# Performance work log

Hardware: AMD Instinct MI355X
Metric: run time of the kernel (lower is better)

## Reference

```python
import jax, jax.numpy as jnp
import numpy as np

B, CLS, C, H, HP, WP, K = 16, 20, 512, 4, 32, 32, 9
G = H * CLS  # grapher channels = 80
EPS = 1e-5
BNS = 1.0 / np.sqrt(1.0 + EPS)  # eval-mode BN, running_mean=0, running_var=1


def _bn(x, g, b, axis):
    shape = [1] * x.ndim
    shape[axis] = -1
    return x * (g * BNS).reshape(shape) + b.reshape(shape)


def setup_inputs():
    key = jax.random.key(0)
    ks = jax.random.split(key, 16)
    def rn(k, shp, scale=0.02):
        return jax.random.normal(k, shp, dtype=jnp.float32) * scale
    return {
        "x_cls": jax.random.normal(ks[0], (B, CLS, C), jnp.float32),
        "x_patch": jax.random.normal(ks[1], (B, C, HP, WP), jnp.float32),
        "norm_x_w": jnp.ones((C, 1, 1), jnp.float32),
        "norm_x_b": jnp.zeros((C, 1, 1), jnp.float32),
        "pq_w": rn(ks[2], (C, C)), "pq_b": rn(ks[3], (C,)),
        "ncls_w": jnp.ones((C,), jnp.float32), "ncls_b": jnp.zeros((C,), jnp.float32),
        "pkv_w": rn(ks[4], (2 * C, C)), "pkv_b": rn(ks[5], (2 * C,)),
        "fc1_w": rn(ks[6], (G, G)), "fc1_b": rn(ks[7], (G,)),
        "bn1_g": jnp.ones((G,), jnp.float32), "bn1_b": jnp.zeros((G,), jnp.float32),
        "mr_w": rn(ks[8], (2 * G, 2 * G // H)), "mr_b": rn(ks[9], (2 * G,)),
        "bn2_g": jnp.ones((2 * G,), jnp.float32), "bn2_b": jnp.zeros((2 * G,), jnp.float32),
        "fc2_w": rn(ks[10], (G, 2 * G)), "fc2_b": rn(ks[11], (G,)),
        "bn3_g": jnp.ones((G,), jnp.float32), "bn3_b": jnp.zeros((G,), jnp.float32),
        "proj_w": rn(ks[12], (C, C)), "proj_b": rn(ks[13], (C,)),
    }


def _forward(x_cls, x_patch, norm_x_w, norm_x_b, pq_w, pq_b, ncls_w, ncls_b,
             pkv_w, pkv_b, fc1_w, fc1_b, bn1_g, bn1_b, mr_w, mr_b, bn2_g, bn2_b,
             fc2_w, fc2_b, bn3_g, bn3_b, proj_w, proj_b):
    hd = C // H
    N = HP * WP
    scale = hd ** -0.5
    # norm_x: LayerNormGeneral over (C,H,W)
    c0 = x_patch - x_patch.mean(axis=(1, 2, 3), keepdims=True)
    s0 = (c0 * c0).mean(axis=(1, 2, 3), keepdims=True)
    xn = c0 / jnp.sqrt(s0 + EPS) * norm_x_w + norm_x_b
    # proj_q (1x1 conv) -> multi-head query [B,H,N,hd]
    q = jnp.einsum('oc,bchw->bohw', pq_w, xn) + pq_b[None, :, None, None]
    q = q.reshape(B, H, hd, N).transpose(0, 1, 3, 2)
    # norm_cls: LayerNorm over channel dim
    m = x_cls.mean(-1, keepdims=True)
    v = ((x_cls - m) ** 2).mean(-1, keepdims=True)
    xc = (x_cls - m) / jnp.sqrt(v + EPS) * ncls_w + ncls_b
    kv = xc @ pkv_w.T + pkv_b                                  # [B,Cls,2C]
    k_, v_ = kv[..., :C], kv[..., C:]
    key_ = k_.reshape(B, CLS, H, hd).transpose(0, 2, 3, 1)     # [B,H,hd,Cls]
    val = v_.reshape(B, CLS, H, hd).transpose(0, 2, 1, 3)      # [B,H,Cls,hd]
    attn = jnp.einsum('bhnd,bhdc->bhnc', q, key_) * scale      # [B,H,N,Cls]
    amap = attn.reshape(B, H, HP, WP, CLS).transpose(0, 1, 4, 2, 3).reshape(B, G, HP, WP)
    # ---- Grapher (ViG gcn_lib): fc1 -> DyGraphConv(MRConv, KNN) -> fc2 -> residual ----
    sc = amap
    x = jnp.einsum('oc,bchw->bohw', fc1_w, amap) + fc1_b[None, :, None, None]
    x = _bn(x, bn1_g, bn1_b, 1)
    xf = x.reshape(B, G, N).transpose(0, 2, 1)                 # [B,N,G]
    # dense KNN on L2-normalized features (indices only, non-diff)
    xu = xf / jnp.maximum(jnp.linalg.norm(xf, axis=-1, keepdims=True), 1e-12)
    sq = jnp.sum(xu * xu, axis=-1)                             # [B,N]
    neg_d = 2.0 * jnp.einsum('bnc,bmc->bnm', xu, xu) - sq[:, :, None] - sq[:, None, :]
    _, nn_idx = jax.lax.top_k(neg_d, K)                        # [B,N,K]
    neigh = xf[jnp.arange(B)[:, None, None], nn_idx]           # [B,N,K,G]
    xj = jnp.max(neigh - xf[:, :, None, :], axis=2)            # [B,N,G] max-relative
    y = jnp.stack([xf, xj], axis=-1).reshape(B, N, 2 * G)      # interleave (x0,xj0,x1,...)
    # grouped 1x1 conv (groups=H), BN, GELU
    yg = y.reshape(B, N, H, 2 * G // H)
    wg = mr_w.reshape(H, 2 * G // H, 2 * G // H)
    z = jnp.einsum('bngi,goi->bngo', yg, wg).reshape(B, N, 2 * G) + mr_b
    z = _bn(z, bn2_g, bn2_b, 2)
    z = jax.nn.gelu(z, approximate=False)
    z2 = z @ fc2_w.T + fc2_b                                   # [B,N,G]
    z2 = _bn(z2, bn3_g, bn3_b, 2)
    gout = z2.transpose(0, 2, 1).reshape(B, G, HP, WP) + sc
    # ---- softmax-weighted value aggregation ----
    attn2 = gout.reshape(B, H, CLS, N).transpose(0, 1, 3, 2)   # [B,H,N,Cls]
    attn2 = jax.nn.softmax(attn2, axis=-1)
    out = jnp.einsum('bhnc,bhcd->bhnd', attn2, val)            # [B,H,N,hd]
    out = out.transpose(0, 1, 3, 2).reshape(B, C, HP, WP)
    out = jnp.einsum('oc,bchw->bohw', proj_w, out) + proj_b[None, :, None, None]
    return x_patch + out


def reference(x_cls, x_patch, norm_x_w, norm_x_b, pq_w, pq_b, ncls_w, ncls_b,
              pkv_w, pkv_b, fc1_w, fc1_b, bn1_g, bn1_b, mr_w, mr_b, bn2_g, bn2_b,
              fc2_w, fc2_b, bn3_g, bn3_b, proj_w, proj_b):
    return _forward(x_cls, x_patch, norm_x_w, norm_x_b, pq_w, pq_b, ncls_w, ncls_b,
                    pkv_w, pkv_b, fc1_w, fc1_b, bn1_g, bn1_b, mr_w, mr_b, bn2_g, bn2_b,
                    fc2_w, fc2_b, bn3_g, bn3_b, proj_w, proj_b)
```

## Files before the change

kernel.cpp:

```cpp
#include <hip/hip_runtime.h>
#include <math.h>

#define DI __device__ __forceinline__

constexpr int B_ = 16, CLS_ = 20, C_ = 512, H_ = 4, HD_ = 128, N_ = 1024, G_ = 80, G2_ = 160, K_ = 9;
constexpr float EPS_ = 1e-5f;
constexpr float BNS_ = 0.9999950000374997f;
constexpr float SCALE_ = 0.08838834764831845f;
constexpr float INVSQRT2_ = 0.7071067811865475f;

typedef __attribute__((ext_vector_type(8))) short bf16x8;
typedef __attribute__((ext_vector_type(4))) float f32x4;

constexpr long OFF_PART  = 0;
constexpr long OFF_STATS = 2048;
constexpr long OFF_EB    = 4096;
constexpr long OFF_EBB   = OFF_EB    + 524288;
constexpr long OFF_KV    = OFF_EBB   + 2048;
constexpr long OFF_AMAPT = OFF_KV    + 327680;
constexpr long OFF_XF    = OFF_AMAPT + 1310720;
constexpr long OFF_XUB   = OFF_XF    + 1310720;
constexpr long OFF_W1BD  = OFF_XUB   + 786432;
constexpr long OFF_FC2B  = OFF_W1BD  + 16384;
constexpr long OFF_SQ    = OFF_FC2B  + 8192;
constexpr long OFF_NEGD  = OFF_SQ    + 16384;
constexpr long OFF_IDX   = OFF_NEGD  + 16777216;
constexpr long OFF_GOUTT = OFF_IDX   + 147456;
constexpr long OFF_WPB   = OFF_GOUTT + 1310720;
constexpr long OFF_Y     = OFF_WPB   + 131072;
constexpr long OFF_AMAPB = OFF_Y     + 1310720;
constexpr long OFF_FC1B  = OFF_AMAPB + 786432;

DI float wsum(float v){
#pragma unroll
  for(int d=1; d<64; d<<=1) v += __shfl_xor(v, d);
  return v;
}
DI unsigned short f2b(float f){
  unsigned u = __float_as_uint(f);
  unsigned r = (u + 0x7FFFu + ((u >> 16) & 1u)) >> 16;
  return (unsigned short)r;
}

#define GLOAD16(g, s) __builtin_amdgcn_global_load_lds((const __attribute__((address_space(1))) void*)(g), \
                        (__attribute__((address_space(3))) void*)(s), 16, 0, 0)

__global__ __launch_bounds__(256) void k_stats_partial(const float* __restrict__ x, float* __restrict__ part){
  int blk = blockIdx.x;
  const float4* xp = (const float4*)x;
  long base4 = (long)blk * 2048;
  int t = threadIdx.x;
  float s = 0.f, ss = 0.f;
#pragma unroll
  for(int j=0;j<8;++j){
    float4 v = xp[base4 + t + 256*j];
    s  += v.x + v.y + v.z + v.w;
    ss += v.x*v.x + v.y*v.y + v.z*v.z + v.w*v.w;
  }
  s = wsum(s); ss = wsum(ss);
  __shared__ float rs[4], rss[4];
  int wv = t >> 6;
  if((t & 63) == 0){ rs[wv] = s; rss[wv] = ss; }
  __syncthreads();
  if(t == 0){
    part[blk*2]   = rs[0]+rs[1]+rs[2]+rs[3];
    part[blk*2+1] = rss[0]+rss[1]+rss[2]+rss[3];
  }
}

__global__ __launch_bounds__(64) void k_stats_final(const float* __restrict__ part, float* __restrict__ stats){
  int b = blockIdx.x, t = threadIdx.x;
  float s  = part[(b*64+t)*2];
  float ss = part[(b*64+t)*2+1];
  s = wsum(s); ss = wsum(ss);
  if(t == 0){
    const float cnt = (float)(C_ * N_);
    float m = s / cnt;
    float var = ss / cnt - m*m;
    stats[b*2]   = m;
    stats[b*2+1] = 1.0f / sqrtf(var + EPS_);
  }
}

__global__ __launch_bounds__(256) void k_xn_t(const float* __restrict__ x, const float* __restrict__ stats,
                                              const float* __restrict__ nw, const float* __restrict__ nb,
                                              unsigned short* __restrict__ xnb){
  __shared__ float tile[64][65];
  int b = blockIdx.z, c0 = blockIdx.y*64, n0 = blockIdx.x*64;
  float m = stats[b*2], inv = stats[b*2+1];
  int t = threadIdx.x;
  const float* xb = x + ((long)b*C_ + c0)*N_ + n0;
#pragma unroll
  for(int j=0;j<4;++j){
    int idx = t + 256*j;
    int r = idx >> 4, c4 = (idx & 15)*4;
    float a = inv * nw[c0+r];
    float bb = nb[c0+r] - m*a;
    float4 v = *(const float4*)&xb[(long)r*N_ + c4];
    tile[r][c4]   = v.x*a + bb;
    tile[r][c4+1] = v.y*a + bb;
    tile[r][c4+2] = v.z*a + bb;
    tile[r][c4+3] = v.w*a + bb;
  }
  __syncthreads();
  unsigned short* ob = xnb + ((long)b*N_ + n0)*C_ + c0;
#pragma unroll
  for(int j=0;j<8;++j){
    int idx = t + 256*j;
    int n = idx >> 5, cc = (idx & 31)*2;
    ushort2 u;
    u.x = f2b(tile[cc][n]);
    u.y = f2b(tile[cc+1][n]);
    *(ushort2*)&ob[(long)n*C_ + cc] = u;
  }
}

__global__ __launch_bounds__(256) void k_wconv(const float* __restrict__ a, unsigned short* __restrict__ oa){
  long i = (long)blockIdx.x*256 + threadIdx.x;
  float4 v = ((const float4*)a)[i];
  uint2 o;
  o.x = (unsigned)f2b(v.x) | ((unsigned)f2b(v.y) << 16);
  o.y = (unsigned)f2b(v.z) | ((unsigned)f2b(v.w) << 16);
  ((uint2*)oa)[i] = o;
}

__global__ __launch_bounds__(256) void k_wsmall(const float* __restrict__ mrw, const float* __restrict__ fc2w,
                                                const float* __restrict__ fc1w,
                                                unsigned short* __restrict__ w1bd, unsigned short* __restrict__ fc2b16,
                                                unsigned short* __restrict__ fc1b16){
  int row = blockIdx.x, t = threadIdx.x;
  if(row < 160){
    if(t < 160){
      unsigned short v = 0;
      if(t/40 == row/40) v = f2b(mrw[row*40 + (t % 40)]);
      w1bd[row*160 + t] = v;
    }
  } else if(row < 240){
    if(t < 160) fc2b16[(row-160)*160 + t] = f2b(fc2w[(long)(row-160)*160 + t]);
  } else {
    int r = row - 240;
    if(t < 96) fc1b16[r*96 + t] = (t < G_) ? f2b(fc1w[(long)r*G_ + t]) : (unsigned short)0;
  }
}

__global__ __launch_bounds__(256) void k_eprep(const float* __restrict__ kv, const float* __restrict__ pqw,
                                               const float* __restrict__ pqb,
                                               unsigned short* __restrict__ Eb, float* __restrict__ ebb){
  int b = blockIdx.x, hh = blockIdx.y, cch = blockIdx.z, t = threadIdx.x;
  if(hh == 4){
    if(cch == 0){
      unsigned* z = (unsigned*)(Eb + ((long)b*128 + 80)*512);
      for(int i=t; i<12288; i+=256) z[i] = 0;
    }
    return;
  }
  int h = hh, c0 = cch*64;
  __shared__ float key[CLS_][HD_];
  __shared__ float part[4][CLS_][64];
  for(int i=t; i<CLS_*HD_; i+=256){
    int cls = i >> 7, d = i & 127;
    key[cls][d] = kv[((long)b*CLS_+cls)*1024 + h*HD_ + d];
  }
  __syncthreads();
  int c = t & 63, ds = t >> 6;
  float acc[CLS_] = {};
  const float* wp = pqw + ((long)(h*HD_ + ds*32))*C_ + c0 + c;
#pragma unroll 8
  for(int di=0; di<32; ++di){
    float wv = wp[(long)di*C_];
#pragma unroll
    for(int cls=0; cls<CLS_; ++cls) acc[cls] += key[cls][ds*32+di]*wv;
  }
#pragma unroll
  for(int cls=0; cls<CLS_; ++cls) part[ds][cls][c] = acc[cls];
  __syncthreads();
  for(int i=t; i<CLS_*64; i+=256){
    int cls = i >> 6, cc = i & 63;
    float v = part[0][cls][cc]+part[1][cls][cc]+part[2][cls][cc]+part[3][cls][cc];
    Eb[((long)b*128 + h*CLS_ + cls)*512 + c0 + cc] = f2b(v*SCALE_);
  }
  if(cch == 0 && t < CLS_){
    float bacc = 0.f;
    for(int d=0; d<HD_; ++d) bacc += key[t][d]*pqb[h*HD_+d];
    ebb[b*G_ + h*CLS_ + t] = bacc*SCALE_;
  }
}

__global__ __launch_bounds__(256) void k_amap_gemm(const unsigned short* __restrict__ Eb,
                                                   const unsigned short* __restrict__ Xb,
                                                   const float* __restrict__ ebb,
                                                   float* __restrict__ amapT,
                                                   unsigned short* __restrict__ amapb){
  __shared__ unsigned short Anl[2048];
  __shared__ unsigned short Bgl[4096];
  int b = blockIdx.y, n0 = blockIdx.x*64;
  int t = threadIdx.x, w = t >> 6, l = t & 63;
  int wr = w >> 1, wc = w & 1;
  f32x4 acc[2][4] = {};
  const unsigned short* At = Xb + ((long)b*N_ + n0 + w*16 + (l>>2))*512 + (l&3)*8;
  const unsigned short* Bt = Eb + ((long)b*128 + w*16 + (l>>2))*512 + (l&3)*8;
  int ra = wr*32 + (l & 15);
  int rb = wc*64 + (l & 15);
  int kq = (l >> 4) * 8;
  for(int k0 = 0; k0 < 512; k0 += 32){
    if(k0) __syncthreads();
    GLOAD16(At + k0,          &Anl[w*512]);
    GLOAD16(Bt + k0,          &Bgl[w*512]);
    GLOAD16(Bt + 64*512 + k0, &Bgl[2048 + w*512]);
    __syncthreads();
    bf16x8 af[2], bfr[4];
#pragma unroll
    for(int rt=0; rt<2; ++rt) af[rt]  = *(const bf16x8*)&Anl[(ra + rt*16)*32 + kq];
#pragma unroll
    for(int ct=0; ct<4; ++ct) bfr[ct] = *(const bf16x8*)&Bgl[(rb + ct*16)*32 + kq];
#pragma unroll
    for(int rt=0; rt<2; ++rt)
#pragma unroll
      for(int ct=0; ct<4; ++ct)
        acc[rt][ct] = __builtin_amdgcn_mfma_f32_16x16x32_bf16(af[rt], bfr[ct], acc[rt][ct], 0, 0, 0);
  }
  int r0 = (l >> 4)*4;
#pragma unroll
  for(int rt=0; rt<2; ++rt){
#pragma unroll
    for(int r=0; r<4; ++r){
      int n = n0 + wr*32 + rt*16 + r0 + r;
      long rowb  = ((long)b*N_ + n)*G_;
      long rowb9 = ((long)b*N_ + n)*96;
#pragma unroll
      for(int ct=0; ct<4; ++ct){
        int g = wc*64 + ct*16 + (l & 15);
        if(g < G_){
          float val = acc[rt][ct][r] + ebb[b*G_ + g];
          amapT[rowb + g] = val;
          amapb[rowb9 + g] = f2b(val);
        } else if(g < 96){
          amapb[rowb9 + g] = 0;
        }
      }
    }
  }
}

template<bool RES>
__global__ __launch_bounds__(256) void k_gemm_mfma(const unsigned short* __restrict__ Wb,
                                                   const unsigned short* __restrict__ Xb,
                                                   const float* __restrict__ bias,
                                                   const float* __restrict__ Res,
                                                   float* __restrict__ Out){
  __shared__ unsigned short Al[4096];
  __shared__ unsigned short Bl[4096];
  int b = blockIdx.z;
  int o0 = blockIdx.y*128, n0 = blockIdx.x*128;
  int t = threadIdx.x, w = t >> 6, l = t & 63;
  int wr = w >> 1, wc = w & 1;
  f32x4 acc[4][4] = {};
  const unsigned short* Wt = Wb + (long)(o0 + w*16 + (l>>2))*512 + (l&3)*8;
  const unsigned short* Xt = Xb + ((long)b*N_ + n0 + w*16 + (l>>2))*512 + (l&3)*8;
  int ra = wr*64 + (l & 15);
  int rb = wc*64 + (l & 15);
  int kq = (l >> 4) * 8;
  for(int k0 = 0; k0 < 512; k0 += 32){
    if(k0) __syncthreads();
    GLOAD16(Wt + k0,            &Al[w*512]);
    GLOAD16(Wt + 64*512 + k0,   &Al[2048 + w*512]);
    GLOAD16(Xt + k0,            &Bl[w*512]);
    GLOAD16(Xt + 64*512 + k0,   &Bl[2048 + w*512]);
    __syncthreads();
    bf16x8 af[4], bfr[4];
#pragma unroll
    for(int i=0;i<4;++i){
      af[i]  = *(const bf16x8*)&Al[(ra + i*16)*32 + kq];
      bfr[i] = *(const bf16x8*)&Bl[(rb + i*16)*32 + kq];
    }
#pragma unroll
    for(int mi=0; mi<4; ++mi)
#pragma unroll
      for(int ni=0; ni<4; ++ni)
        acc[mi][ni] = __builtin_amdgcn_mfma_f32_16x16x32_bf16(af[mi], bfr[ni], acc[mi][ni], 0, 0, 0);
  }
  long obase = ((long)b*C_ + o0 + wr*64)*N_ + n0 + wc*64 + (l & 15);
  int r0 = (l >> 4) * 4;
#pragma unroll
  for(int mi=0; mi<4; ++mi){
#pragma unroll
    for(int r=0; r<4; ++r){
      int row = mi*16 + r0 + r;
      float bi = bias[o0 + wr*64 + row];
#pragma unroll
      for(int ni=0; ni<4; ++ni){
        long oi = obase + (long)row*N_ + ni*16;
        float v = acc[mi][ni][r] + bi;
        if(RES) v += Res[oi];
        Out[oi] = v;
      }
    }
  }
}

__global__ __launch_bounds__(256) void k_cls_kv(const float* __restrict__ xcls,
                                                const float* __restrict__ ncw, const float* __restrict__ ncb,
                                                const float* __restrict__ pkvw, const float* __restrict__ pkvb,
                                                float* __restrict__ kv){
  int b = blockIdx.x;
  int ochunk = blockIdx.y;
  __shared__ float xc[CLS_][C_];
  int t = threadIdx.x, wv = t >> 6, l = t & 63;
  for(int cls = wv; cls < CLS_; cls += 4){
    const float* xr = xcls + ((long)b*CLS_ + cls) * C_;
    float vals[8];
    float s = 0.f, ss = 0.f;
#pragma unroll
    for(int j=0;j<8;++j){ float v = xr[l + 64*j]; vals[j] = v; s += v; ss += v*v; }
    s = wsum(s); ss = wsum(ss);
    float m = s / (float)C_;
    float var = ss / (float)C_ - m*m;
    float inv = 1.0f / sqrtf(var + EPS_);
#pragma unroll
    for(int j=0;j<8;++j){
      int c = l + 64*j;
      xc[cls][c] = (vals[j]-m)*inv*ncw[c] + ncb[c];
    }
  }
  __syncthreads();
  int o = ochunk*128 + (t & 127);
  int cls0 = (t >> 7) * 10;
  float acc[10] = {};
  const float* wrow = pkvw + (long)o * C_;
  for(int k4 = 0; k4 < C_; k4 += 4){
    float4 w4 = *(const float4*)&wrow[k4];
#pragma unroll
    for(int i=0;i<10;++i){
      acc[i] += w4.x*xc[cls0+i][k4] + w4.y*xc[cls0+i][k4+1] + w4.z*xc[cls0+i][k4+2] + w4.w*xc[cls0+i][k4+3];
    }
  }
  float bo = pkvb[o];
#pragma unroll
  for(int i=0;i<10;++i) kv[((long)b*CLS_ + cls0+i)*1024 + o] = acc[i] + bo;
}

__global__ __launch_bounds__(256) void k_fc1_mfma(const unsigned short* __restrict__ amapb,
                                                  const unsigned short* __restrict__ w1b,
                                                  const float* __restrict__ bias,
                                                  const float* __restrict__ g1, const float* __restrict__ b1,
                                                  float* __restrict__ xf, unsigned short* __restrict__ xub,
                                                  float* __restrict__ sq){
  int t = threadIdx.x, w = t >> 6, l = t & 63;
  long row0 = ((long)blockIdx.x*4 + w)*16;
  int lr = l & 15, lk = l >> 4;
  bf16x8 ay[3];
  const unsigned short* arow = amapb + (row0 + lr)*96 + lk*8;
#pragma unroll
  for(int ks=0; ks<3; ++ks) ay[ks] = *(const bf16x8*)&arow[ks*32];
  f32x4 acc[5] = {};
  const unsigned short* wrow = w1b + (long)lr*96 + lk*8;
#pragma unroll
  for(int ks=0; ks<3; ++ks){
#pragma unroll
    for(int ct=0; ct<5; ++ct){
      bf16x8 bw = *(const bf16x8*)&wrow[ct*16*96 + ks*32];
      acc[ct] = __builtin_amdgcn_mfma_f32_16x16x32_bf16(ay[ks], bw, acc[ct], 0, 0, 0);
    }
  }
  float v[5][4];
  float ssq[4] = {0.f,0.f,0.f,0.f};
#pragma unroll
  for(int ct=0; ct<5; ++ct){
    int o = ct*16 + lr;
    float bi = bias[o], ga = g1[o]*BNS_, bb = b1[o];
#pragma unroll
    for(int i=0;i<4;++i){
      float vv = (acc[ct][i] + bi)*ga + bb;
      v[ct][i] = vv;
      ssq[i] += vv*vv;
    }
  }
#pragma unroll
  for(int d=1; d<16; d<<=1){
#pragma unroll
    for(int i=0;i<4;++i) ssq[i] += __shfl_xor(ssq[i], d);
  }
#pragma unroll
  for(int i=0;i<4;++i){
    long row = row0 + lk*4 + i;
    float invn = 1.0f / fmaxf(sqrtf(ssq[i]), 1e-12f);
#pragma unroll
    for(int ct=0; ct<5; ++ct){
      int o = ct*16 + lr;
      xf[row*G_ + o] = v[ct][i];
      xub[row*96 + o] = f2b(v[ct][i]*invn);
    }
    xub[row*96 + 80 + lr] = 0;
    if(lr == 0) sq[row] = ssq[i]*invn*invn;
  }
}

__global__ __launch_bounds__(256) void k_negd_mfma(const unsigned short* __restrict__ xub,
                                                   const float* __restrict__ sq,
                                                   float* __restrict__ negd){
  __shared__ unsigned short Al[128*96];
  __shared__ unsigned short Bl[128*96];
  int b = blockIdx.z;
  int n0 = blockIdx.y*128, m0 = blockIdx.x*128;
  int t = threadIdx.x, w = t >> 6, l = t & 63;
  int wr = w >> 1, wc = w & 1;
  const unsigned short* gA = xub + ((long)b*N_ + n0)*96;
  const unsigned short* gB = xub + ((long)b*N_ + m0)*96;
#pragma unroll
  for(int rd=0; rd<6; ++rd){
    int chunk = rd*4 + w;
    GLOAD16(gA + chunk*512 + l*8, &Al[chunk*512]);
    GLOAD16(gB + chunk*512 + l*8, &Bl[chunk*512]);
  }
  __syncthreads();
  f32x4 acc[4][4] = {};
  int ra = wr*64 + (l & 15);
  int rb = wc*64 + (l & 15);
#pragma unroll
  for(int ks=0; ks<3; ++ks){
    int kq = ks*32 + (l >> 4)*8;
    bf16x8 af[4], bfr[4];
#pragma unroll
    for(int i=0;i<4;++i){
      af[i]  = *(const bf16x8*)&Al[(ra + i*16)*96 + kq];
      bfr[i] = *(const bf16x8*)&Bl[(rb + i*16)*96 + kq];
    }
#pragma unroll
    for(int mi=0; mi<4; ++mi)
#pragma unroll
      for(int ni=0; ni<4; ++ni)
        acc[mi][ni] = __builtin_amdgcn_mfma_f32_16x16x32_bf16(af[mi], bfr[ni], acc[mi][ni], 0, 0, 0);
  }
  int r0 = (l >> 4)*4;
  const float* sqb = sq + (long)b*N_;
#pragma unroll
  for(int mi=0; mi<4; ++mi){
#pragma unroll
    for(int r=0; r<4; ++r){
      int n = n0 + wr*64 + mi*16 + r0 + r;
      float sn = sqb[n];
      long row = ((long)b*N_ + n)*N_;
#pragma unroll
      for(int ni=0; ni<4; ++ni){
        int m = m0 + wc*64 + ni*16 + (l & 15);
        negd[row + m] = 2.f*acc[mi][ni][r] - sn - sqb[m];
      }
    }
  }
}

__global__ __launch_bounds__(256) void k_topk(const float* __restrict__ negd, int* __restrict__ idx){
  int t = threadIdx.x, wv = t >> 6, l = t & 63;
  long r = (long)blockIdx.x*4 + wv;
  const float* row = negd + r*N_;
  float vals[16];
#pragma unroll
  for(int j=0;j<16;++j) vals[j] = row[l + 64*j];
#pragma unroll
  for(int p=0; p<K_; ++p){
    float bv = vals[0]; int bj = 0;
#pragma unroll
    for(int j=1;j<16;++j) if(vals[j] > bv){ bv = vals[j]; bj = j; }
    int bm = l + 64*bj;
#pragma unroll
    for(int d=1; d<64; d<<=1){
      float ov = __shfl_xor(bv, d);
      int   om = __shfl_xor(bm, d);
      if(ov > bv || (ov == bv && om < bm)){ bv = ov; bm = om; }
    }
#pragma unroll
    for(int j=0;j<16;++j) if(bm == l + 64*j) vals[j] = -INFINITY;
    if(l == 0) idx[r*K_ + p] = bm;
  }
}

__global__ __launch_bounds__(256) void k_y(const float* __restrict__ xf, const int* __restrict__ idx,
                                           unsigned short* __restrict__ y){
  int t = threadIdx.x, wv = t >> 6, l = t & 63;
  long r = (long)blockIdx.x*4 + wv;
  long b = r >> 10;
  const float* frow = xf + r*G_;
  int o2s = (l < 16) ? (64 + l) : 0;
  float f0 = frow[l];
  float f1 = frow[o2s];
  const int* ixp = idx + r*K_;
  float m0 = -INFINITY, m1 = -INFINITY;
#pragma unroll
  for(int k=0;k<K_;++k){
    const float* nr = xf + ((long)b*N_ + ixp[k])*G_;
    m0 = fmaxf(m0, nr[l]);
    m1 = fmaxf(m1, nr[o2s]);
  }
  unsigned short* yr = y + r*G2_;
  ushort2 u0; u0.x = f2b(f0); u0.y = f2b(m0 - f0);
  *(ushort2*)&yr[2*l] = u0;
  if(l < 16){
    ushort2 u1; u1.x = f2b(f1); u1.y = f2b(m1 - f1);
    *(ushort2*)&yr[128 + 2*l] = u1;
  }
}

__global__ __launch_bounds__(256) void k_mixer_mfma(const unsigned short* __restrict__ y,
                                                    const unsigned short* __restrict__ w1bd,
                                                    const float* __restrict__ mrb,
                                                    const float* __restrict__ g2, const float* __restrict__ b2,
                                                    const unsigned short* __restrict__ fc2b16,
                                                    const float* __restrict__ fc2bias,
                                                    const float* __restrict__ g3, const float* __restrict__ b3,
                                                    const float* __restrict__ amapT, float* __restrict__ goutT){
  __shared__ unsigned short zl[4][16][G2_];
  int t = threadIdx.x, w = t >> 6, l = t & 63;
  long row0 = ((long)blockIdx.x*4 + w)*16;
  int lr = l & 15, lk = l >> 4;
  bf16x8 ay[5];
  const unsigned short* yrow = y + (row0 + lr)*G2_ + lk*8;
#pragma unroll
  for(int ks=0; ks<5; ++ks) ay[ks] = *(const bf16x8*)&yrow[ks*32];
  f32x4 accz[10] = {};
  const unsigned short* wb = w1bd + (long)lr*G2_ + lk*8;
#pragma unroll
  for(int ks=0; ks<5; ++ks){
#pragma unroll
    for(int ct=0; ct<10; ++ct){
      bf16x8 bw = *(const bf16x8*)&wb[ct*16*G2_ + ks*32];
      accz[ct] = __builtin_amdgcn_mfma_f32_16x16x32_bf16(ay[ks], bw, accz[ct], 0, 0, 0);
    }
  }
#pragma unroll
  for(int ct=0; ct<10; ++ct){
    int o = ct*16 + lr;
    float bi = mrb[o], ga = g2[o]*BNS_, bb = b2[o];
#pragma unroll
    for(int i=0;i<4;++i){
      float v = (accz[ct][i] + bi)*ga + bb;
      float zz = v * 0.5f * (1.0f + erff(v * INVSQRT2_));
      zl[w][lk*4 + i][o] = f2b(zz);
    }
  }
  __syncthreads();
  bf16x8 az[5];
#pragma unroll
  for(int ks=0; ks<5; ++ks) az[ks] = *(const bf16x8*)&zl[w][lr][ks*32 + lk*8];
  f32x4 acc2[5] = {};
  const unsigned short* fb = fc2b16 + (long)lr*G2_ + lk*8;
#pragma unroll
  for(int ks=0; ks<5; ++ks){
#pragma unroll
    for(int ct=0; ct<5; ++ct){
      bf16x8 bw = *(const bf16x8*)&fb[ct*16*G2_ + ks*32];
      acc2[ct] = __builtin_amdgcn_mfma_f32_16x16x32_bf16(az[ks], bw, acc2[ct], 0, 0, 0);
    }
  }
#pragma unroll
  for(int ct=0; ct<5; ++ct){
    int o = ct*16 + lr;
    float bi = fc2bias[o], ga = g3[o]*BNS_, bb = b3[o];
#pragma unroll
    for(int i=0;i<4;++i){
      long row = row0 + lk*4 + i;
      float v = (acc2[ct][i] + bi)*ga + bb + amapT[row*G_ + o];
      goutT[row*G_ + o] = v;
    }
  }
}

__global__ __launch_bounds__(256) void k_softmax_pv(const float* __restrict__ goutT, const float* __restrict__ kv,
                                                    unsigned short* __restrict__ aob){
  int bh = blockIdx.x; int b = bh >> 2, h = bh & 3;
  int n0 = blockIdx.y * 64;
  __shared__ unsigned short Vt[128*32];
  __shared__ unsigned short Pl[64*40];
  __shared__ unsigned short Os[64*132];
  int t = threadIdx.x, w = t >> 6, l = t & 63;
  if(t < 128){
    int d = t;
    const float* vb = kv + ((long)b*CLS_)*1024 + C_ + h*HD_ + d;
#pragma unroll
    for(int cls=0; cls<CLS_; ++cls) Vt[d*32+cls] = f2b(vb[(long)cls*1024]);
#pragma unroll
    for(int cls=CLS_; cls<32; ++cls) Vt[d*32+cls] = 0;
  }
  if(t < 64){
    int n = n0 + t;
    const float* gr = goutT + ((long)b*N_ + n)*G_ + h*CLS_;
    float x[CLS_];
    float mx = -INFINITY;
#pragma unroll
    for(int cls=0; cls<CLS_; ++cls){ x[cls] = gr[cls]; mx = fmaxf(mx, x[cls]); }
    float s = 0.f;
#pragma unroll
    for(int cls=0; cls<CLS_; ++cls){ x[cls] = expf(x[cls]-mx); s += x[cls]; }
    float inv = 1.0f / s;
#pragma unroll
    for(int cls=0; cls<CLS_; ++cls) Pl[t*40+cls] = f2b(x[cls]*inv);
#pragma unroll
    for(int cls=CLS_; cls<32; ++cls) Pl[t*40+cls] = 0;
  }
  __syncthreads();
  int lr = l & 15, kq = (l >> 4)*8;
  f32x4 acc[4][2] = {};
  bf16x8 af[4], bf2[2];
#pragma unroll
  for(int rt=0; rt<4; ++rt) af[rt] = *(const bf16x8*)&Pl[(rt*16+lr)*40 + kq];
#pragma unroll
  for(int ci=0; ci<2; ++ci) bf2[ci] = *(const bf16x8*)&Vt[((2*w+ci)*16+lr)*32 + kq];
#pragma unroll
  for(int rt=0; rt<4; ++rt)
#pragma unroll
    for(int ci=0; ci<2; ++ci)
      acc[rt][ci] = __builtin_amdgcn_mfma_f32_16x16x32_bf16(af[rt], bf2[ci], acc[rt][ci], 0, 0, 0);
  int r0 = (l >> 4)*4;
#pragma unroll
  for(int rt=0; rt<4; ++rt)
#pragma unroll
    for(int ci=0; ci<2; ++ci)
#pragma unroll
      for(int i=0; i<4; ++i)
        Os[(rt*16 + r0 + i)*132 + (2*w+ci)*16 + lr] = f2b(acc[rt][ci][i]);
  __syncthreads();
  unsigned short* ob = aob + ((long)b*N_ + n0)*C_ + h*HD_;
#pragma unroll
  for(int j=0; j<8; ++j){
    int idx = t + 256*j;
    int row = idx >> 5, ch = idx & 31;
    *(ushort4*)&ob[(long)row*C_ + ch*4] =
        *(const ushort4*)&Os[row*132 + ch*4];
  }
}

extern "C" void kernel_launch(void* const* d_in, const int* in_sizes, int n_in,
                              void* d_out, int out_size, void* d_ws, size_t ws_size,
                              hipStream_t stream){
  const float* x_cls   = (const float*)d_in[0];
  const float* x_patch = (const float*)d_in[1];
  const float* norm_x_w = (const float*)d_in[2];
  const float* norm_x_b = (const float*)d_in[3];
  const float* pq_w  = (const float*)d_in[4];
  const float* pq_b  = (const float*)d_in[5];
  const float* ncls_w = (const float*)d_in[6];
  const float* ncls_b = (const float*)d_in[7];
  const float* pkv_w = (const float*)d_in[8];
  const float* pkv_b = (const float*)d_in[9];
  const float* fc1_w = (const float*)d_in[10];
  const float* fc1_b = (const float*)d_in[11];
  const float* bn1_g = (const float*)d_in[12];
  const float* bn1_b = (const float*)d_in[13];
  const float* mr_w  = (const float*)d_in[14];
  const float* mr_b  = (const float*)d_in[15];
  const float* bn2_g = (const float*)d_in[16];
  const float* bn2_b = (const float*)d_in[17];
  const float* fc2_w = (const float*)d_in[18];
  const float* fc2_b = (const float*)d_in[19];
  const float* bn3_g = (const float*)d_in[20];
  const float* bn3_b = (const float*)d_in[21];
  const float* proj_w = (const float*)d_in[22];
  const float* proj_b = (const float*)d_in[23];

  float* ws = (float*)d_ws;
  float* part   = ws + OFF_PART;
  float* stats  = ws + OFF_STATS;
  float* ebb    = ws + OFF_EBB;
  float* kvbuf  = ws + OFF_KV;
  float* amapT  = ws + OFF_AMAPT;
  float* xf     = ws + OFF_XF;
  float* sqbuf  = ws + OFF_SQ;
  float* negd   = ws + OFF_NEGD;
  int*   idxbuf = (int*)(ws + OFF_IDX);
  float* goutT  = ws + OFF_GOUTT;
  unsigned short* Eb     = (unsigned short*)(ws + OFF_EB);
  unsigned short* xub    = (unsigned short*)(ws + OFF_XUB);
  unsigned short* w1bd   = (unsigned short*)(ws + OFF_W1BD);
  unsigned short* fc2b16 = (unsigned short*)(ws + OFF_FC2B);
  unsigned short* ybuf   = (unsigned short*)(ws + OFF_Y);
  unsigned short* amapb  = (unsigned short*)(ws + OFF_AMAPB);
  unsigned short* fc1b16 = (unsigned short*)(ws + OFF_FC1B);
  unsigned short* xnb = (unsigned short*)(ws + OFF_NEGD);
  unsigned short* aob = (unsigned short*)(ws + OFF_NEGD);
  unsigned short* wpb = (unsigned short*)(ws + OFF_WPB);
  float* out = (float*)d_out;

  k_stats_partial<<<1024, 256, 0, stream>>>(x_patch, part);
  k_stats_final<<<16, 64, 0, stream>>>(part, stats);
  k_xn_t<<<dim3(16,8,16), 256, 0, stream>>>(x_patch, stats, norm_x_w, norm_x_b, xnb);
  k_cls_kv<<<dim3(16,8), 256, 0, stream>>>(x_cls, ncls_w, ncls_b, pkv_w, pkv_b, kvbuf);
  k_eprep<<<dim3(16,5,8), 256, 0, stream>>>(kvbuf, pq_w, pq_b, Eb, ebb);
  k_wconv<<<256, 256, 0, stream>>>(proj_w, wpb);
  k_wsmall<<<320, 256, 0, stream>>>(mr_w, fc2_w, fc1_w, w1bd, fc2b16, fc1b16);
  k_amap_gemm<<<dim3(16,16), 256, 0, stream>>>(Eb, xnb, ebb, amapT, amapb);
  k_fc1_mfma<<<256, 256, 0, stream>>>(amapb, fc1b16, fc1_b, bn1_g, bn1_b, xf, xub, sqbuf);
  k_negd_mfma<<<dim3(8,8,16), 256, 0, stream>>>(xub, sqbuf, negd);
  k_topk<<<4096, 256, 0, stream>>>(negd, idxbuf);
  k_y<<<4096, 256, 0, stream>>>(xf, idxbuf, ybuf);
  k_mixer_mfma<<<256, 256, 0, stream>>>(ybuf, w1bd, mr_b, bn2_g, bn2_b,
                                        fc2b16, fc2_b, bn3_g, bn3_b, amapT, goutT);
  k_softmax_pv<<<dim3(64,16), 256, 0, stream>>>(goutT, kvbuf, aob);
  k_gemm_mfma<true><<<dim3(8,4,16), 256, 0, stream>>>(wpb, aob, proj_b, x_patch, out);
}
```

Before: 194.7 us.

## Fold LayerNorm into query weights and fuse topk with neighbor gather

The per-sample LayerNorm scale and shift of x_patch are folded into the E matrix and an extra per-sample bias term, so the amap GEMM reads raw x_patch and converts it to bf16 in LDS. This removes the separate normalise-and-transpose kernel and its bf16 intermediate round trip. The topk and neighbor-max kernels are merged so indices stay in registers, and the two weight-conversion kernels are combined into one launch. The trade-off is a 66KB LDS tile in the GEMM, which lowers occupancy, uncoalesced transposing stores into LDS, and bf16 rounding of raw rather than normalised values.

```diff
diff --git a/kernel.cpp b/kernel.cpp
--- a/kernel.cpp
+++ b/kernel.cpp
@@ -24,12 +24,12 @@
 constexpr long OFF_FC2B  = OFF_W1BD  + 16384;
 constexpr long OFF_SQ    = OFF_FC2B  + 8192;
 constexpr long OFF_NEGD  = OFF_SQ    + 16384;
-constexpr long OFF_IDX   = OFF_NEGD  + 16777216;
-constexpr long OFF_GOUTT = OFF_IDX   + 147456;
+constexpr long OFF_GOUTT = OFF_NEGD  + 16777216 + 147456;
 constexpr long OFF_WPB   = OFF_GOUTT + 1310720;
 constexpr long OFF_Y     = OFF_WPB   + 131072;
 constexpr long OFF_AMAPB = OFF_Y     + 1310720;
 constexpr long OFF_FC1B  = OFF_AMAPB + 786432;
+constexpr long OFF_PB    = OFF_FC1B  + 4096;
 
 DI float wsum(float v){
 #pragma unroll
@@ -82,53 +82,22 @@
   }
 }
 
-__global__ __launch_bounds__(256) void k_xn_t(const float* __restrict__ x, const float* __restrict__ stats,
-                                              const float* __restrict__ nw, const float* __restrict__ nb,
-                                              unsigned short* __restrict__ xnb){
-  __shared__ float tile[64][65];
-  int b = blockIdx.z, c0 = blockIdx.y*64, n0 = blockIdx.x*64;
-  float m = stats[b*2], inv = stats[b*2+1];
-  int t = threadIdx.x;
-  const float* xb = x + ((long)b*C_ + c0)*N_ + n0;
-#pragma unroll
-  for(int j=0;j<4;++j){
-    int idx = t + 256*j;
-    int r = idx >> 4, c4 = (idx & 15)*4;
-    float a = inv * nw[c0+r];
-    float bb = nb[c0+r] - m*a;
-    float4 v = *(const float4*)&xb[(long)r*N_ + c4];
-    tile[r][c4]   = v.x*a + bb;
-    tile[r][c4+1] = v.y*a + bb;
-    tile[r][c4+2] = v.z*a + bb;
-    tile[r][c4+3] = v.w*a + bb;
-  }
-  __syncthreads();
-  unsigned short* ob = xnb + ((long)b*N_ + n0)*C_ + c0;
-#pragma unroll
-  for(int j=0;j<8;++j){
-    int idx = t + 256*j;
-    int n = idx >> 5, cc = (idx & 31)*2;
-    ushort2 u;
-    u.x = f2b(tile[cc][n]);
-    u.y = f2b(tile[cc+1][n]);
-    *(ushort2*)&ob[(long)n*C_ + cc] = u;
-  }
-}
-
-__global__ __launch_bounds__(256) void k_wconv(const float* __restrict__ a, unsigned short* __restrict__ oa){
-  long i = (long)blockIdx.x*256 + threadIdx.x;
-  float4 v = ((const float4*)a)[i];
-  uint2 o;
-  o.x = (unsigned)f2b(v.x) | ((unsigned)f2b(v.y) << 16);
-  o.y = (unsigned)f2b(v.z) | ((unsigned)f2b(v.w) << 16);
-  ((uint2*)oa)[i] = o;
-}
-
-__global__ __launch_bounds__(256) void k_wsmall(const float* __restrict__ mrw, const float* __restrict__ fc2w,
-                                                const float* __restrict__ fc1w,
-                                                unsigned short* __restrict__ w1bd, unsigned short* __restrict__ fc2b16,
-                                                unsigned short* __restrict__ fc1b16){
-  int row = blockIdx.x, t = threadIdx.x;
+__global__ __launch_bounds__(256) void k_wprep(const float* __restrict__ projw, unsigned short* __restrict__ wpb,
+                                               const float* __restrict__ mrw, const float* __restrict__ fc2w,
+                                               const float* __restrict__ fc1w,
+                                               unsigned short* __restrict__ w1bd, unsigned short* __restrict__ fc2b16,
+                                               unsigned short* __restrict__ fc1b16){
+  int blk = blockIdx.x, t = threadIdx.x;
+  if(blk < 256){
+    long i = (long)blk*256 + t;
+    float4 v = ((const float4*)projw)[i];
+    uint2 o;
+    o.x = (unsigned)f2b(v.x) | ((unsigned)f2b(v.y) << 16);
+    o.y = (unsigned)f2b(v.z) | ((unsigned)f2b(v.w) << 16);
+    ((uint2*)wpb)[i] = o;
+    return;
+  }
+  int row = blk - 256;
   if(row < 160){
     if(t < 160){
       unsigned short v = 0;
@@ -144,8 +113,10 @@
 }
 
 __global__ __launch_bounds__(256) void k_eprep(const float* __restrict__ kv, const float* __restrict__ pqw,
-                                               const float* __restrict__ pqb,
-                                               unsigned short* __restrict__ Eb, float* __restrict__ ebb){
+                                               const float* __restrict__ pqb, const float* __restrict__ stats,
+                                               const float* __restrict__ nw, const float* __restrict__ nbv,
+                                               unsigned short* __restrict__ Eb, float* __restrict__ ebb,
+                                               float* __restrict__ pb){
   int b = blockIdx.x, hh = blockIdx.y, cch = blockIdx.z, t = threadIdx.x;
   if(hh == 4){
     if(cch == 0){
@@ -155,6 +126,7 @@
     return;
   }
   int h = hh, c0 = cch*64;
+  float m = stats[b*2], inv = stats[b*2+1];
   __shared__ float key[CLS_][HD_];
   __shared__ float part[4][CLS_][64];
   for(int i=t; i<CLS_*HD_; i+=256){
@@ -176,41 +148,72 @@
   __syncthreads();
   for(int i=t; i<CLS_*64; i+=256){
     int cls = i >> 6, cc = i & 63;
-    float v = part[0][cls][cc]+part[1][cls][cc]+part[2][cls][cc]+part[3][cls][cc];
-    Eb[((long)b*128 + h*CLS_ + cls)*512 + c0 + cc] = f2b(v*SCALE_);
-  }
-  if(cch == 0 && t < CLS_){
+    float v = (part[0][cls][cc]+part[1][cls][cc]+part[2][cls][cc]+part[3][cls][cc]) * SCALE_;
+    int cg = c0 + cc;
+    float a = inv * nw[cg];
+    float bbv = nbv[cg] - m*a;
+    Eb[((long)b*128 + h*CLS_ + cls)*512 + cg] = f2b(v*a);
+    part[0][cls][cc] = v*bbv;
+  }
+  __syncthreads();
+  if(t < CLS_){
+    float s = 0.f;
+    for(int cc=0; cc<64; ++cc) s += part[0][t][cc];
+    pb[((long)b*8 + cch)*G_ + h*CLS_ + t] = s;
+  }
+  if(cch == 0 && t >= 64 && t < 64 + CLS_){
+    int tt = t - 64;
     float bacc = 0.f;
-    for(int d=0; d<HD_; ++d) bacc += key[t][d]*pqb[h*HD_+d];
-    ebb[b*G_ + h*CLS_ + t] = bacc*SCALE_;
+    for(int d=0; d<HD_; ++d) bacc += key[tt][d]*pqb[h*HD_+d];
+    ebb[b*G_ + h*CLS_ + tt] = bacc*SCALE_;
   }
 }
 
 __global__ __launch_bounds__(256) void k_amap_gemm(const unsigned short* __restrict__ Eb,
-                                                   const unsigned short* __restrict__ Xb,
+                                                   const float* __restrict__ xp,
                                                    const float* __restrict__ ebb,
+                                                   const float* __restrict__ pb,
                                                    float* __restrict__ amapT,
                                                    unsigned short* __restrict__ amapb){
-  __shared__ unsigned short Anl[2048];
+  __shared__ unsigned short Xl[64*520];
   __shared__ unsigned short Bgl[4096];
   int b = blockIdx.y, n0 = blockIdx.x*64;
   int t = threadIdx.x, w = t >> 6, l = t & 63;
   int wr = w >> 1, wc = w & 1;
+  {
+    int nb = t & 7, cl = t >> 3;
+    const float* xb = xp + (long)b*C_*N_ + n0 + nb*8;
+#pragma unroll 4
+    for(int pass=0; pass<16; ++pass){
+      int c = pass*32 + cl;
+      const float* src = xb + (long)c*N_;
+      float4 v0 = *(const float4*)src;
+      float4 v1 = *(const float4*)(src+4);
+      int base = (nb*8)*520 + c;
+      Xl[base         ] = f2b(v0.x);
+      Xl[base + 520   ] = f2b(v0.y);
+      Xl[base + 520*2 ] = f2b(v0.z);
+      Xl[base + 520*3 ] = f2b(v0.w);
+      Xl[base + 520*4 ] = f2b(v1.x);
+      Xl[base + 520*5 ] = f2b(v1.y);
+      Xl[base + 520*6 ] = f2b(v1.z);
+      Xl[base + 520*7 ] = f2b(v1.w);
+    }
+  }
+  __syncthreads();
   f32x4 acc[2][4] = {};
-  const unsigned short* At = Xb + ((long)b*N_ + n0 + w*16 + (l>>2))*512 + (l&3)*8;
   const unsigned short* Bt = Eb + ((long)b*128 + w*16 + (l>>2))*512 + (l&3)*8;
   int ra = wr*32 + (l & 15);
   int rb = wc*64 + (l & 15);
   int kq = (l >> 4) * 8;
   for(int k0 = 0; k0 < 512; k0 += 32){
     if(k0) __syncthreads();
-    GLOAD16(At + k0,          &Anl[w*512]);
     GLOAD16(Bt + k0,          &Bgl[w*512]);
     GLOAD16(Bt + 64*512 + k0, &Bgl[2048 + w*512]);
     __syncthreads();
     bf16x8 af[2], bfr[4];
 #pragma unroll
-    for(int rt=0; rt<2; ++rt) af[rt]  = *(const bf16x8*)&Anl[(ra + rt*16)*32 + kq];
+    for(int rt=0; rt<2; ++rt) af[rt]  = *(const bf16x8*)&Xl[(ra + rt*16)*520 + k0 + kq];
 #pragma unroll
     for(int ct=0; ct<4; ++ct) bfr[ct] = *(const bf16x8*)&Bgl[(rb + ct*16)*32 + kq];
 #pragma unroll
@@ -218,6 +221,18 @@
 #pragma unroll
       for(int ct=0; ct<4; ++ct)
         acc[rt][ct] = __builtin_amdgcn_mfma_f32_16x16x32_bf16(af[rt], bfr[ct], acc[rt][ct], 0, 0, 0);
+  }
+  float bias4[4];
+#pragma unroll
+  for(int ct=0; ct<4; ++ct){
+    int g = wc*64 + ct*16 + (l & 15);
+    float bi = 0.f;
+    if(g < G_){
+      bi = ebb[b*G_ + g];
+#pragma unroll
+      for(int cc=0; cc<8; ++cc) bi += pb[((long)b*8 + cc)*G_ + g];
+    }
+    bias4[ct] = bi;
   }
   int r0 = (l >> 4)*4;
 #pragma unroll
@@ -231,7 +246,7 @@
       for(int ct=0; ct<4; ++ct){
         int g = wc*64 + ct*16 + (l & 15);
         if(g < G_){
-          float val = acc[rt][ct][r] + ebb[b*G_ + g];
+          float val = acc[rt][ct][r] + bias4[ct];
           amapT[rowb + g] = val;
           amapb[rowb9 + g] = f2b(val);
         } else if(g < 96){
@@ -449,13 +464,16 @@
   }
 }
 
-__global__ __launch_bounds__(256) void k_topk(const float* __restrict__ negd, int* __restrict__ idx){
+__global__ __launch_bounds__(256) void k_topk_y(const float* __restrict__ negd, const float* __restrict__ xf,
+                                                unsigned short* __restrict__ y){
   int t = threadIdx.x, wv = t >> 6, l = t & 63;
   long r = (long)blockIdx.x*4 + wv;
+  long b = r >> 10;
   const float* row = negd + r*N_;
   float vals[16];
 #pragma unroll
   for(int j=0;j<16;++j) vals[j] = row[l + 64*j];
+  int nbs[K_];
 #pragma unroll
   for(int p=0; p<K_; ++p){
     float bv = vals[0]; int bj = 0;
@@ -468,26 +486,18 @@
       int   om = __shfl_xor(bm, d);
       if(ov > bv || (ov == bv && om < bm)){ bv = ov; bm = om; }
     }
+    nbs[p] = bm;
 #pragma unroll
     for(int j=0;j<16;++j) if(bm == l + 64*j) vals[j] = -INFINITY;
-    if(l == 0) idx[r*K_ + p] = bm;
-  }
-}
-
-__global__ __launch_bounds__(256) void k_y(const float* __restrict__ xf, const int* __restrict__ idx,
-                                           unsigned short* __restrict__ y){
-  int t = threadIdx.x, wv = t >> 6, l = t & 63;
-  long r = (long)blockIdx.x*4 + wv;
-  long b = r >> 10;
+  }
   const float* frow = xf + r*G_;
   int o2s = (l < 16) ? (64 + l) : 0;
   float f0 = frow[l];
   float f1 = frow[o2s];
-  const int* ixp = idx + r*K_;
   float m0 = -INFINITY, m1 = -INFINITY;
 #pragma unroll
   for(int k=0;k<K_;++k){
-    const float* nr = xf + ((long)b*N_ + ixp[k])*G_;
+    const float* nr = xf + ((long)b*N_ + nbs[k])*G_;
     m0 = fmaxf(m0, nr[l]);
     m1 = fmaxf(m1, nr[o2s]);
   }
@@ -665,8 +675,8 @@
   float* xf     = ws + OFF_XF;
   float* sqbuf  = ws + OFF_SQ;
   float* negd   = ws + OFF_NEGD;
-  int*   idxbuf = (int*)(ws + OFF_IDX);
   float* goutT  = ws + OFF_GOUTT;
+  float* pbuf   = ws + OFF_PB;
   unsigned short* Eb     = (unsigned short*)(ws + OFF_EB);
   unsigned short* xub    = (unsigned short*)(ws + OFF_XUB);
   unsigned short* w1bd   = (unsigned short*)(ws + OFF_W1BD);
@@ -674,23 +684,19 @@
   unsigned short* ybuf   = (unsigned short*)(ws + OFF_Y);
   unsigned short* amapb  = (unsigned short*)(ws + OFF_AMAPB);
   unsigned short* fc1b16 = (unsigned short*)(ws + OFF_FC1B);
-  unsigned short* xnb = (unsigned short*)(ws + OFF_NEGD);
   unsigned short* aob = (unsigned short*)(ws + OFF_NEGD);
   unsigned short* wpb = (unsigned short*)(ws + OFF_WPB);
   float* out = (float*)d_out;
 
   k_stats_partial<<<1024, 256, 0, stream>>>(x_patch, part);
   k_stats_final<<<16, 64, 0, stream>>>(part, stats);
-  k_xn_t<<<dim3(16,8,16), 256, 0, stream>>>(x_patch, stats, norm_x_w, norm_x_b, xnb);
   k_cls_kv<<<dim3(16,8), 256, 0, stream>>>(x_cls, ncls_w, ncls_b, pkv_w, pkv_b, kvbuf);
-  k_eprep<<<dim3(16,5,8), 256, 0, stream>>>(kvbuf, pq_w, pq_b, Eb, ebb);
-  k_wconv<<<256, 256, 0, stream>>>(proj_w, wpb);
-  k_wsmall<<<320, 256, 0, stream>>>(mr_w, fc2_w, fc1_w, w1bd, fc2b16, fc1b16);
-  k_amap_gemm<<<dim3(16,16), 256, 0, stream>>>(Eb, xnb, ebb, amapT, amapb);
+  k_eprep<<<dim3(16,5,8), 256, 0, stream>>>(kvbuf, pq_w, pq_b, stats, norm_x_w, norm_x_b, Eb, ebb, pbuf);
+  k_wprep<<<576, 256, 0, stream>>>(proj_w, wpb, mr_w, fc2_w, fc1_w, w1bd, fc2b16, fc1b16);
+  k_amap_gemm<<<dim3(16,16), 256, 0, stream>>>(Eb, x_patch, ebb, pbuf, amapT, amapb);
   k_fc1_mfma<<<256, 256, 0, stream>>>(amapb, fc1b16, fc1_b, bn1_g, bn1_b, xf, xub, sqbuf);
   k_negd_mfma<<<dim3(8,8,16), 256, 0, stream>>>(xub, sqbuf, negd);
-  k_topk<<<4096, 256, 0, stream>>>(negd, idxbuf);
-  k_y<<<4096, 256, 0, stream>>>(xf, idxbuf, ybuf);
+  k_topk_y<<<4096, 256, 0, stream>>>(negd, xf, ybuf);
   k_mixer_mfma<<<256, 256, 0, stream>>>(ybuf, w1bd, mr_b, bn2_g, bn2_b,
                                         fc2b16, fc2_b, bn3_g, bn3_b, amapT, goutT);
   k_softmax_pv<<<dim3(64,16), 256, 0, stream>>>(goutT, kvbuf, aob);
```

New measurement: 181.4 us. 1.07x faster.
